# Kernel optimization log

Hardware: AMD Instinct MI355X
Metric: run time of the kernel (lower is better)

Reference implementation:

```python
import jax, jax.numpy as jnp
import numpy as np

N_USER = 80000
N_ITEM = 20000
N = N_USER + N_ITEM          # total nodes
E = 1600000                  # edges (nnz of norm_adj), avg degree 16
EMB = 64                     # emb_size
FEAT = 64                    # feature_dim -> input_dim = 128
D = EMB + FEAT               # 128
L = 3                        # number of GCN layers, layer_size=[128,128,128]
K = 3                        # max_hop
B = 4096                     # batch_size


def setup_inputs() -> dict:
    key = jax.random.key(0)
    ks = jax.random.split(key, 16)
    deg_scale = 1.0 / 16.0  # ~normalized adjacency values
    return {
        'edge_row': jax.random.randint(ks[0], (E,), 0, N, dtype=jnp.int32),
        'edge_col': jax.random.randint(ks[1], (E,), 0, N, dtype=jnp.int32),
        'edge_val': jax.random.uniform(ks[2], (E,), dtype=jnp.float32) * deg_scale,
        'feat': jax.random.normal(ks[3], (N_USER, FEAT), dtype=jnp.float32) * 0.1,
        'user_emb': jax.random.normal(ks[4], (N_USER, EMB), dtype=jnp.float32) * 0.1,
        'item_emb1': jax.random.normal(ks[5], (N_ITEM, EMB), dtype=jnp.float32) * 0.1,
        'item_emb2': jax.random.normal(ks[6], (N_ITEM, FEAT), dtype=jnp.float32) * 0.1,
        'alphas': jax.random.normal(ks[7], (L, K), dtype=jnp.float32) * 0.1,
        'W_gc': jax.random.normal(ks[8], (L, D, D), dtype=jnp.float32) * 0.05,
        'b_gc': jax.random.normal(ks[9], (L, 1, D), dtype=jnp.float32) * 0.05,
        'W_bi': jax.random.normal(ks[10], (L, D, D), dtype=jnp.float32) * 0.05,
        'b_bi': jax.random.normal(ks[11], (L, 1, D), dtype=jnp.float32) * 0.05,
        'users': jax.random.randint(ks[12], (B,), 0, N_USER, dtype=jnp.int32),
        'pos_items': jax.random.randint(ks[13], (B,), 0, N_ITEM, dtype=jnp.int32),
        'neg_items': jax.random.randint(ks[14], (B,), 0, N_ITEM, dtype=jnp.int32),
    }


def reference(edge_row, edge_col, edge_val, feat, user_emb, item_emb1,
              item_emb2, alphas, W_gc, b_gc, W_bi, b_bi,
              users, pos_items, neg_items):
    def spmm(X):
        # A_hat @ X via edge-list gather + segment-sum (sparse.mm equivalent)
        return jax.ops.segment_sum(edge_val[:, None] * X[edge_col], edge_row,
                                   num_segments=N)

    # ego embeddings: [[user_emb|feat], [item_emb1|item_emb2]] -> [N, D]
    ego = jnp.concatenate([
        jnp.concatenate([user_emb, item_emb1], axis=0),
        jnp.concatenate([feat, item_emb2], axis=0),
    ], axis=1)

    all_embs = [ego]
    for k in range(L):
        # multi-order aggregation: sum_i beta_i * A^i @ ego
        beta = jax.nn.softmax(alphas[k])
        cur = spmm(ego)
        side = beta[0] * cur
        for i in range(1, K):
            cur = spmm(cur)
            side = side + beta[i] * cur
        sum_e = side @ W_gc[k] + b_gc[k]
        bi_e = (ego * side) @ W_bi[k] + b_bi[k]
        # aggregator_mode == 'sum_bi'
        ego = jax.nn.leaky_relu(sum_e, negative_slope=0.2) + bi_e
        # mess_dropout = 0 -> identity; L2-normalize rows (F.normalize eps=1e-12)
        norm = ego / jnp.maximum(
            jnp.linalg.norm(ego, axis=1, keepdims=True), 1e-12)
        all_embs.append(norm)

    all_emb = jnp.concatenate(all_embs, axis=1)  # [N, D*(L+1)] = [N, 512]
    u_emb = all_emb[:N_USER]
    i_emb = all_emb[N_USER:]
    return (u_emb[users], i_emb[pos_items], i_emb[neg_items])
```

## Files before the change

kernel.cpp:

```cpp
#include <hip/hip_runtime.h>
#include <hip/hip_bf16.h>

typedef __hip_bfloat16 hbf16;
typedef unsigned short u16;
typedef __bf16 bf16x8 __attribute__((ext_vector_type(8)));
typedef float f32x4 __attribute__((ext_vector_type(4)));

#define N_USERS 80000
#define N_ITEMS 20000
#define NTOT    100000
#define NEDGE   1600000
#define DDIM    128
#define NLAY    3
#define KHOP    3
#define NB      4096
#define LBM     128
#define NBUK    49
#define BROWS   2048

__device__ inline u16 f2bfu(float f) { __bf16 h = (__bf16)f; return __builtin_bit_cast(u16, h); }

__global__ void beta_kernel(const float* __restrict__ alphas, float* __restrict__ beta) {
    if (threadIdx.x == 0 && blockIdx.x == 0) {
        for (int k = 0; k < NLAY; ++k) {
            float a[KHOP];
            float m = -1e30f;
            for (int i = 0; i < KHOP; ++i) { a[i] = alphas[k*KHOP+i]; m = fmaxf(m, a[i]); }
            float s = 0.f;
            for (int i = 0; i < KHOP; ++i) { a[i] = expf(a[i] - m); s += a[i]; }
            for (int i = 0; i < KHOP; ++i) beta[k*KHOP+i] = a[i] / s;
        }
    }
}

__global__ void build_ego_kernel(const float* __restrict__ feat, const float* __restrict__ user_emb,
                                 const float* __restrict__ item_emb1, const float* __restrict__ item_emb2,
                                 u16* __restrict__ ego) {
    int i = blockIdx.x * 256 + threadIdx.x;
    int n = i >> 7, d = i & 127;
    float v;
    if (n < N_USERS) {
        v = (d < 64) ? user_emb[n*64 + d] : feat[n*64 + d - 64];
    } else {
        int m = n - N_USERS;
        v = (d < 64) ? item_emb1[m*64 + d] : item_emb2[m*64 + d - 64];
    }
    ego[i] = f2bfu(v);
}

__global__ void transpose_w_kernel(const float* __restrict__ Wgc, const float* __restrict__ Wbi,
                                   u16* __restrict__ WTgc, u16* __restrict__ WTbi) {
    __shared__ float t[32][33];
    int z = blockIdx.z;
    const float* W = (z < 3) ? (Wgc + (size_t)z * 16384) : (Wbi + (size_t)(z - 3) * 16384);
    u16* WT = (z < 3) ? (WTgc + (size_t)z * 16384) : (WTbi + (size_t)(z - 3) * 16384);
    int r0 = blockIdx.y * 32, c0 = blockIdx.x * 32;
    for (int i = threadIdx.y; i < 32; i += 8)
        t[i][threadIdx.x] = W[(size_t)(r0 + i) * 128 + c0 + threadIdx.x];
    __syncthreads();
    for (int i = threadIdx.y; i < 32; i += 8)
        WT[(size_t)(c0 + i) * 128 + r0 + threadIdx.x] = f2bfu(t[threadIdx.x][i]);
}

__global__ void zero_kernel(int* __restrict__ p, int n) {
    int i = blockIdx.x * 256 + threadIdx.x;
    if (i < n) p[i] = 0;
}

__global__ __launch_bounds__(256) void bhist_kernel(const int* __restrict__ er,
                                                    int* __restrict__ bbins) {
    __shared__ int l[NBUK];
    int tid = threadIdx.x;
    if (tid < NBUK) l[tid] = 0;
    __syncthreads();
    for (int i = blockIdx.x * 256 + tid; i < NEDGE; i += gridDim.x * 256)
        atomicAdd(&l[er[i] >> 11], 1);
    __syncthreads();
    if (tid < NBUK && l[tid]) atomicAdd(&bbins[tid], l[tid]);
}

__global__ void bscan_kernel(const int* __restrict__ bbins, int* __restrict__ bbase,
                             int* __restrict__ bcur) {
    if (threadIdx.x == 0 && blockIdx.x == 0) {
        int acc = 0;
        for (int b = 0; b < NBUK; ++b) { int t = bbins[b]; bbase[b] = acc; bcur[b] = acc; acc += t; }
        bbase[NBUK] = acc;
    }
}

__global__ __launch_bounds__(256) void bappend_kernel(
    const int* __restrict__ er, const int* __restrict__ ec, const float* __restrict__ ev,
    int* __restrict__ bcur, int* __restrict__ tmprow, int2* __restrict__ tmpcv) {
    __shared__ int lcnt[NBUK], lbase[NBUK], lrank[NBUK];
    int tid = threadIdx.x;
    for (int b = tid; b < NBUK; b += 256) { lcnt[b] = 0; lrank[b] = 0; }
    __syncthreads();
    int base = blockIdx.x * 2048;
    int r[8], c[8], vb[8], bk[8];
    bool ok[8];
    #pragma unroll
    for (int k = 0; k < 8; ++k) {
        int i = base + k * 256 + tid;
        ok[k] = i < NEDGE;
        bk[k] = 0;
        if (ok[k]) {
            r[k] = er[i]; c[k] = ec[i]; vb[k] = __float_as_int(ev[i]);
            bk[k] = r[k] >> 11;
            atomicAdd(&lcnt[bk[k]], 1);
        }
    }
    __syncthreads();
    for (int b = tid; b < NBUK; b += 256)
        lbase[b] = lcnt[b] ? atomicAdd(&bcur[b], lcnt[b]) : 0;
    __syncthreads();
    #pragma unroll
    for (int k = 0; k < 8; ++k) {
        if (ok[k]) {
            int rank = atomicAdd(&lrank[bk[k]], 1);
            int pos = lbase[bk[k]] + rank;
            tmprow[pos] = r[k];
            tmpcv[pos] = make_int2(c[k], vb[k]);
        }
    }
}

__global__ __launch_bounds__(1024) void bfinal_kernel(
    const int* __restrict__ bbase, const int* __restrict__ tmprow,
    const int2* __restrict__ tmpcv, int* __restrict__ rowptr, int2* __restrict__ edges) {
    __shared__ int lhist[BROWS];
    __shared__ int lbase[BROWS];
    __shared__ int s2[1024];
    int b = blockIdx.x, tid = threadIdx.x;
    int s = bbase[b], e = bbase[b + 1];
    int rbase = b << 11;
    int nrows = min(NTOT - rbase, BROWS);
    lhist[tid] = 0; lhist[tid + 1024] = 0;
    __syncthreads();
    for (int i = s + tid; i < e; i += 1024)
        atomicAdd(&lhist[tmprow[i] - rbase], 1);
    __syncthreads();
    int a0 = lhist[tid * 2], a1 = lhist[tid * 2 + 1];
    s2[tid] = a0 + a1;
    __syncthreads();
    for (int off = 1; off < 1024; off <<= 1) {
        int t = (tid >= off) ? s2[tid - off] : 0;
        __syncthreads();
        s2[tid] += t;
        __syncthreads();
    }
    int excl = s2[tid] - a0 - a1;
    lbase[tid * 2] = excl;
    lbase[tid * 2 + 1] = excl + a0;
    __syncthreads();
    for (int j = tid; j < nrows; j += 1024)
        rowptr[rbase + j] = s + lbase[j];
    if (b == NBUK - 1 && tid == 0) rowptr[NTOT] = NEDGE;
    lhist[tid * 2] = lbase[tid * 2];
    lhist[tid * 2 + 1] = lbase[tid * 2 + 1];
    __syncthreads();
    for (int i = s + tid; i < e; i += 1024) {
        int lr = tmprow[i] - rbase;
        int p = atomicAdd(&lhist[lr], 1);
        edges[s + p] = tmpcv[i];
    }
}

__device__ inline void ld_edge_nt(const int2* __restrict__ p, int& c, float& v) {
    unsigned long long rec =
        __builtin_nontemporal_load(reinterpret_cast<const unsigned long long*>(p));
    c = (int)(unsigned)(rec & 0xffffffffull);
    v = __int_as_float((int)(unsigned)(rec >> 32));
}

__global__ __launch_bounds__(256) void spmm_kernel(
    const int* __restrict__ rowptr, const int2* __restrict__ edges,
    const u16* __restrict__ X, u16* __restrict__ Y) {
    int tid = threadIdx.x;
    int r = blockIdx.x * 16 + (tid >> 4);
    int lane = tid & 15;
    int s = rowptr[r], e = rowptr[r + 1];
    float acc[8];
    #pragma unroll
    for (int i = 0; i < 8; ++i) acc[i] = 0.f;
    const u16* xb = X + lane * 8;
    int j = s;
    for (; j + 8 <= e; j += 8) {
        int cc[8]; float vv[8];
        #pragma unroll
        for (int u = 0; u < 8; ++u) ld_edge_nt(edges + j + u, cc[u], vv[u]);
        bf16x8 x[8];
        #pragma unroll
        for (int u = 0; u < 8; ++u)
            x[u] = *reinterpret_cast<const bf16x8*>(xb + (size_t)cc[u] * DDIM);
        #pragma unroll
        for (int u = 0; u < 8; ++u) {
            #pragma unroll
            for (int i = 0; i < 8; ++i) acc[i] = fmaf(vv[u], (float)x[u][i], acc[i]);
        }
    }
    for (; j + 4 <= e; j += 4) {
        int cc[4]; float vv[4];
        #pragma unroll
        for (int u = 0; u < 4; ++u) ld_edge_nt(edges + j + u, cc[u], vv[u]);
        bf16x8 x0 = *reinterpret_cast<const bf16x8*>(xb + (size_t)cc[0] * DDIM);
        bf16x8 x1 = *reinterpret_cast<const bf16x8*>(xb + (size_t)cc[1] * DDIM);
        bf16x8 x2 = *reinterpret_cast<const bf16x8*>(xb + (size_t)cc[2] * DDIM);
        bf16x8 x3 = *reinterpret_cast<const bf16x8*>(xb + (size_t)cc[3] * DDIM);
        #pragma unroll
        for (int i = 0; i < 8; ++i) acc[i] = fmaf(vv[0], (float)x0[i], acc[i]);
        #pragma unroll
        for (int i = 0; i < 8; ++i) acc[i] = fmaf(vv[1], (float)x1[i], acc[i]);
        #pragma unroll
        for (int i = 0; i < 8; ++i) acc[i] = fmaf(vv[2], (float)x2[i], acc[i]);
        #pragma unroll
        for (int i = 0; i < 8; ++i) acc[i] = fmaf(vv[3], (float)x3[i], acc[i]);
    }
    for (; j < e; ++j) {
        int cc; float vv;
        ld_edge_nt(edges + j, cc, vv);
        bf16x8 x = *reinterpret_cast<const bf16x8*>(xb + (size_t)cc * DDIM);
        #pragma unroll
        for (int i = 0; i < 8; ++i) acc[i] = fmaf(vv, (float)x[i], acc[i]);
    }
    size_t oi = (size_t)r * DDIM + lane * 8;
    bf16x8 y;
    #pragma unroll
    for (int i = 0; i < 8; ++i) y[i] = (__bf16)acc[i];
    *reinterpret_cast<bf16x8*>(Y + oi) = y;
}

__global__ __launch_bounds__(512) void layer_kernel(
    const u16* __restrict__ ego, const u16* __restrict__ h1,
    const u16* __restrict__ h2, const u16* __restrict__ h3,
    const float* __restrict__ beta3,
    const u16* __restrict__ wtgc, const u16* __restrict__ wtbi,
    const float* __restrict__ bgc, const float* __restrict__ bbi,
    u16* __restrict__ ego_out, u16* __restrict__ normbuf) {
    __shared__ __align__(16) unsigned char smem[131072];
    const int AS = 0, AB = 32768, WG = 65536, WB = 98304;
    int tid = threadIdx.x;
    int base = blockIdx.x * LBM;
    float b0 = beta3[0], b1 = beta3[1], b2 = beta3[2];

    {
        int row = tid >> 2, q = tid & 3;
        int grow = base + row;
        bool ok = grow < NTOT;
        size_t roff = (size_t)grow * DDIM + q * 32;
        int sw = (row & 7) << 4;
        #pragma unroll
        for (int cg = 0; cg < 4; ++cg) {
            bf16x8 pa, pb;
            if (ok) {
                bf16x8 x1 = *reinterpret_cast<const bf16x8*>(h1 + roff + cg * 8);
                bf16x8 x2 = *reinterpret_cast<const bf16x8*>(h2 + roff + cg * 8);
                bf16x8 x3 = *reinterpret_cast<const bf16x8*>(h3 + roff + cg * 8);
                bf16x8 ev = *reinterpret_cast<const bf16x8*>(ego + roff + cg * 8);
                #pragma unroll
                for (int i = 0; i < 8; ++i) {
                    float sf = b0 * (float)x1[i] + b1 * (float)x2[i] + b2 * (float)x3[i];
                    pa[i] = (__bf16)sf;
                    pb[i] = (__bf16)(sf * (float)ev[i]);
                }
            } else {
                #pragma unroll
                for (int i = 0; i < 8; ++i) { pa[i] = (__bf16)0.f; pb[i] = (__bf16)0.f; }
            }
            int kb = q * 64 + cg * 16;
            *reinterpret_cast<bf16x8*>(&smem[AS + row * 256 + (kb ^ sw)]) = pa;
            *reinterpret_cast<bf16x8*>(&smem[AB + row * 256 + (kb ^ sw)]) = pb;
        }
    }
    #pragma unroll
    for (int p = 0; p < 4; ++p) {
        int slot = tid + p * 512;
        int n = slot >> 4, ks = slot & 15;
        uint4 g  = *reinterpret_cast<const uint4*>(wtgc + n * DDIM + ks * 8);
        uint4 bq = *reinterpret_cast<const uint4*>(wtbi + n * DDIM + ks * 8);
        int addr = n * 256 + ((ks * 16) ^ ((n & 7) << 4));
        *reinterpret_cast<uint4*>(&smem[WG + addr]) = g;
        *reinterpret_cast<uint4*>(&smem[WB + addr]) = bq;
    }
    __syncthreads();

    int l = tid & 63, w = tid >> 6;
    int m = l & 15, g16 = l >> 4;
    int sw = (m & 7) << 4;
    int arow = (w * 16 + m) * 256;
    f32x4 accg[8], accb[8];
    #pragma unroll
    for (int nt = 0; nt < 8; ++nt) {
        accg[nt] = (f32x4){0.f, 0.f, 0.f, 0.f};
        accb[nt] = (f32x4){0.f, 0.f, 0.f, 0.f};
    }
    #pragma unroll
    for (int kk = 0; kk < 4; ++kk) {
        int ka = (kk * 64 + g16 * 16) ^ sw;
        bf16x8 as = *reinterpret_cast<const bf16x8*>(&smem[AS + arow + ka]);
        bf16x8 ab = *reinterpret_cast<const bf16x8*>(&smem[AB + arow + ka]);
        #pragma unroll
        for (int nt = 0; nt < 8; ++nt) {
            int na = (nt * 16 + m) * 256 + ka;
            bf16x8 bg = *reinterpret_cast<const bf16x8*>(&smem[WG + na]);
            accg[nt] = __builtin_amdgcn_mfma_f32_16x16x32_bf16(as, bg, accg[nt], 0, 0, 0);
            bf16x8 bb = *reinterpret_cast<const bf16x8*>(&smem[WB + na]);
            accb[nt] = __builtin_amdgcn_mfma_f32_16x16x32_bf16(ab, bb, accb[nt], 0, 0, 0);
        }
    }
    float bgv[8], bbv[8];
    #pragma unroll
    for (int nt = 0; nt < 8; ++nt) { bgv[nt] = bgc[nt * 16 + m]; bbv[nt] = bbi[nt * 16 + m]; }
    float vv[8][4];
    float ss[4] = {0.f, 0.f, 0.f, 0.f};
    #pragma unroll
    for (int nt = 0; nt < 8; ++nt) {
        #pragma unroll
        for (int rr = 0; rr < 4; ++rr) {
            float se = accg[nt][rr] + bgv[nt];
            float be = accb[nt][rr] + bbv[nt];
            float v = (se > 0.f ? se : 0.2f * se) + be;
            vv[nt][rr] = v;
            ss[rr] += v * v;
            int row = base + w * 16 + g16 * 4 + rr;
            if (row < NTOT) ego_out[(size_t)row * DDIM + nt * 16 + m] = f2bfu(v);
        }
    }
    #pragma unroll
    for (int rr = 0; rr < 4; ++rr) {
        ss[rr] += __shfl_xor(ss[rr], 1, 64);
        ss[rr] += __shfl_xor(ss[rr], 2, 64);
        ss[rr] += __shfl_xor(ss[rr], 4, 64);
        ss[rr] += __shfl_xor(ss[rr], 8, 64);
        ss[rr] = 1.f / fmaxf(sqrtf(ss[rr]), 1e-12f);
    }
    #pragma unroll
    for (int nt = 0; nt < 8; ++nt) {
        #pragma unroll
        for (int rr = 0; rr < 4; ++rr) {
            int row = base + w * 16 + g16 * 4 + rr;
            if (row < NTOT) normbuf[(size_t)row * DDIM + nt * 16 + m] = f2bfu(vv[nt][rr] * ss[rr]);
        }
    }
}

__global__ void gather_ego_kernel(const float* __restrict__ feat, const float* __restrict__ user_emb,
                                  const float* __restrict__ item_emb1, const float* __restrict__ item_emb2,
                                  const int* __restrict__ users, const int* __restrict__ pos,
                                  const int* __restrict__ neg, float* __restrict__ out) {
    int i = blockIdx.x * 256 + threadIdx.x;
    int which = i / (NB * DDIM);
    int rem = i - which * (NB * DDIM);
    int b = rem >> 7, d = rem & 127;
    float v;
    if (which == 0) {
        int u = users[b];
        v = (d < 64) ? user_emb[u*64 + d] : feat[u*64 + d - 64];
    } else {
        int m = (which == 1) ? pos[b] : neg[b];
        v = (d < 64) ? item_emb1[m*64 + d] : item_emb2[m*64 + d - 64];
    }
    out[(size_t)which * NB * 512 + (size_t)b * 512 + d] = v;
}

__global__ void gather_slice_kernel(const u16* __restrict__ src, const int* __restrict__ users,
                                    const int* __restrict__ pos, const int* __restrict__ neg,
                                    float* __restrict__ out, int slot) {
    int i = blockIdx.x * 256 + threadIdx.x;
    int which = i / (NB * DDIM);
    int rem = i - which * (NB * DDIM);
    int b = rem >> 7, c = rem & 127;
    int row;
    if (which == 0)      row = users[b];
    else if (which == 1) row = N_USERS + pos[b];
    else                 row = N_USERS + neg[b];
    unsigned int u = src[(size_t)row * DDIM + c];
    out[(size_t)which * NB * 512 + (size_t)b * 512 + slot * 128 + c] =
        __builtin_bit_cast(float, u << 16);
}

extern "C" void kernel_launch(void* const* d_in, const int* in_sizes, int n_in,
                              void* d_out, int out_size, void* d_ws, size_t ws_size,
                              hipStream_t stream) {
    (void)in_sizes; (void)n_in; (void)out_size; (void)ws_size;
    const int*   edge_row  = (const int*)  d_in[0];
    const int*   edge_col  = (const int*)  d_in[1];
    const float* edge_val  = (const float*)d_in[2];
    const float* feat      = (const float*)d_in[3];
    const float* user_emb  = (const float*)d_in[4];
    const float* item_emb1 = (const float*)d_in[5];
    const float* item_emb2 = (const float*)d_in[6];
    const float* alphas    = (const float*)d_in[7];
    const float* W_gc      = (const float*)d_in[8];
    const float* b_gc      = (const float*)d_in[9];
    const float* W_bi      = (const float*)d_in[10];
    const float* b_bi      = (const float*)d_in[11];
    const int*   users     = (const int*)  d_in[12];
    const int*   pos_items = (const int*)  d_in[13];
    const int*   neg_items = (const int*)  d_in[14];
    float* out = (float*)d_out;

    char* ws = (char*)d_ws;
    size_t off = 0;
    auto alloc = [&](size_t bytes) -> char* {
        char* p = ws + off;
        off = (off + bytes + 255) & ~(size_t)255;
        return p;
    };
    u16*   ego      = (u16*)  alloc((size_t)NTOT * DDIM * 2);
    u16*   h1       = (u16*)  alloc((size_t)NTOT * DDIM * 2);
    u16*   h2       = (u16*)  alloc((size_t)NTOT * DDIM * 2);
    u16*   h3       = (u16*)  alloc((size_t)NTOT * DDIM * 2);
    u16*   normbuf  = (u16*)  alloc((size_t)NTOT * DDIM * 2);
    int*   rowptr   = (int*)  alloc((size_t)(NTOT + 1) * 4);
    int*   bbins    = (int*)  alloc((NBUK + 2) * 4);
    int*   bbase    = (int*)  alloc((NBUK + 2) * 4);
    int*   bcur     = (int*)  alloc((NBUK + 2) * 4);
    int2*  edges    = (int2*) alloc((size_t)NEDGE * 8);
    u16*   wtgc     = (u16*)  alloc((size_t)NLAY * DDIM * DDIM * 2);
    u16*   wtbi     = (u16*)  alloc((size_t)NLAY * DDIM * DDIM * 2);
    float* beta     = (float*)alloc(256);

    int*  tmprow = (int*)h1;
    int2* tmpcv  = (int2*)((char*)h1 + (size_t)NEDGE * 4);

    beta_kernel<<<1, 64, 0, stream>>>(alphas, beta);
    build_ego_kernel<<<(NTOT * DDIM) / 256, 256, 0, stream>>>(feat, user_emb, item_emb1, item_emb2, ego);
    transpose_w_kernel<<<dim3(4, 4, 6), dim3(32, 8), 0, stream>>>(W_gc, W_bi, wtgc, wtbi);

    zero_kernel<<<1, 64, 0, stream>>>(bbins, NBUK);
    bhist_kernel<<<512, 256, 0, stream>>>(edge_row, bbins);
    bscan_kernel<<<1, 64, 0, stream>>>(bbins, bbase, bcur);
    bappend_kernel<<<(NEDGE + 2047) / 2048, 256, 0, stream>>>(edge_row, edge_col, edge_val,
                                                              bcur, tmprow, tmpcv);
    bfinal_kernel<<<NBUK, 1024, 0, stream>>>(bbase, tmprow, tmpcv, rowptr, edges);

    gather_ego_kernel<<<(3 * NB * DDIM) / 256, 256, 0, stream>>>(feat, user_emb, item_emb1, item_emb2,
                                                                 users, pos_items, neg_items, out);

    int lgrid = (NTOT + LBM - 1) / LBM;
    for (int k = 0; k < NLAY; ++k) {
        spmm_kernel<<<NTOT / 16, 256, 0, stream>>>(rowptr, edges, ego, h1);
        spmm_kernel<<<NTOT / 16, 256, 0, stream>>>(rowptr, edges, h1, h2);
        spmm_kernel<<<NTOT / 16, 256, 0, stream>>>(rowptr, edges, h2, h3);
        layer_kernel<<<lgrid, 512, 0, stream>>>(ego, h1, h2, h3, beta + 3 * k,
                                                wtgc + (size_t)k * DDIM * DDIM, wtbi + (size_t)k * DDIM * DDIM,
                                                b_gc + (size_t)k * DDIM, b_bi + (size_t)k * DDIM,
                                                ego, normbuf);
        gather_slice_kernel<<<(3 * NB * DDIM) / 256, 256, 0, stream>>>(normbuf, users, pos_items, neg_items, out, k + 1);
    }
}
```

Measured before the change: 875.6 us.

## Load GEMM A operands directly into registers, halve LDS, add SpMM sched barriers

The layer kernel no longer stages the beta-combined side and ego*side tiles in shared memory. Each lane now loads its MFMA A-fragment straight from global memory and combines it in registers, which halves LDS use to 64KB and adds a launch-bounds hint for more resident blocks. The SpMM kernel gains sched_barrier calls so all gathers issue before the FMAs, and its 4-edge tail loop is restructured the same way. The risk is less coalesced global loads for the A operand and more register pressure.

```diff
diff --git a/kernel.cpp b/kernel.cpp
--- a/kernel.cpp
+++ b/kernel.cpp
@@ -192,6 +192,7 @@
         #pragma unroll
         for (int u = 0; u < 8; ++u)
             x[u] = *reinterpret_cast<const bf16x8*>(xb + (size_t)cc[u] * DDIM);
+        __builtin_amdgcn_sched_barrier(0);
         #pragma unroll
         for (int u = 0; u < 8; ++u) {
             #pragma unroll
@@ -202,18 +203,16 @@
         int cc[4]; float vv[4];
         #pragma unroll
         for (int u = 0; u < 4; ++u) ld_edge_nt(edges + j + u, cc[u], vv[u]);
-        bf16x8 x0 = *reinterpret_cast<const bf16x8*>(xb + (size_t)cc[0] * DDIM);
-        bf16x8 x1 = *reinterpret_cast<const bf16x8*>(xb + (size_t)cc[1] * DDIM);
-        bf16x8 x2 = *reinterpret_cast<const bf16x8*>(xb + (size_t)cc[2] * DDIM);
-        bf16x8 x3 = *reinterpret_cast<const bf16x8*>(xb + (size_t)cc[3] * DDIM);
-        #pragma unroll
-        for (int i = 0; i < 8; ++i) acc[i] = fmaf(vv[0], (float)x0[i], acc[i]);
-        #pragma unroll
-        for (int i = 0; i < 8; ++i) acc[i] = fmaf(vv[1], (float)x1[i], acc[i]);
-        #pragma unroll
-        for (int i = 0; i < 8; ++i) acc[i] = fmaf(vv[2], (float)x2[i], acc[i]);
-        #pragma unroll
-        for (int i = 0; i < 8; ++i) acc[i] = fmaf(vv[3], (float)x3[i], acc[i]);
+        bf16x8 x[4];
+        #pragma unroll
+        for (int u = 0; u < 4; ++u)
+            x[u] = *reinterpret_cast<const bf16x8*>(xb + (size_t)cc[u] * DDIM);
+        __builtin_amdgcn_sched_barrier(0);
+        #pragma unroll
+        for (int u = 0; u < 4; ++u) {
+            #pragma unroll
+            for (int i = 0; i < 8; ++i) acc[i] = fmaf(vv[u], (float)x[u][i], acc[i]);
+        }
     }
     for (; j < e; ++j) {
         int cc; float vv;
@@ -229,48 +228,19 @@
     *reinterpret_cast<bf16x8*>(Y + oi) = y;
 }
 
-__global__ __launch_bounds__(512) void layer_kernel(
+__global__ __launch_bounds__(512, 4) void layer_kernel(
     const u16* __restrict__ ego, const u16* __restrict__ h1,
     const u16* __restrict__ h2, const u16* __restrict__ h3,
     const float* __restrict__ beta3,
     const u16* __restrict__ wtgc, const u16* __restrict__ wtbi,
     const float* __restrict__ bgc, const float* __restrict__ bbi,
     u16* __restrict__ ego_out, u16* __restrict__ normbuf) {
-    __shared__ __align__(16) unsigned char smem[131072];
-    const int AS = 0, AB = 32768, WG = 65536, WB = 98304;
+    __shared__ __align__(16) unsigned char smem[65536];
+    const int WG = 0, WB = 32768;
     int tid = threadIdx.x;
     int base = blockIdx.x * LBM;
     float b0 = beta3[0], b1 = beta3[1], b2 = beta3[2];
 
-    {
-        int row = tid >> 2, q = tid & 3;
-        int grow = base + row;
-        bool ok = grow < NTOT;
-        size_t roff = (size_t)grow * DDIM + q * 32;
-        int sw = (row & 7) << 4;
-        #pragma unroll
-        for (int cg = 0; cg < 4; ++cg) {
-            bf16x8 pa, pb;
-            if (ok) {
-                bf16x8 x1 = *reinterpret_cast<const bf16x8*>(h1 + roff + cg * 8);
-                bf16x8 x2 = *reinterpret_cast<const bf16x8*>(h2 + roff + cg * 8);
-                bf16x8 x3 = *reinterpret_cast<const bf16x8*>(h3 + roff + cg * 8);
-                bf16x8 ev = *reinterpret_cast<const bf16x8*>(ego + roff + cg * 8);
-                #pragma unroll
-                for (int i = 0; i < 8; ++i) {
-                    float sf = b0 * (float)x1[i] + b1 * (float)x2[i] + b2 * (float)x3[i];
-                    pa[i] = (__bf16)sf;
-                    pb[i] = (__bf16)(sf * (float)ev[i]);
-                }
-            } else {
-                #pragma unroll
-                for (int i = 0; i < 8; ++i) { pa[i] = (__bf16)0.f; pb[i] = (__bf16)0.f; }
-            }
-            int kb = q * 64 + cg * 16;
-            *reinterpret_cast<bf16x8*>(&smem[AS + row * 256 + (kb ^ sw)]) = pa;
-            *reinterpret_cast<bf16x8*>(&smem[AB + row * 256 + (kb ^ sw)]) = pb;
-        }
-    }
     #pragma unroll
     for (int p = 0; p < 4; ++p) {
         int slot = tid + p * 512;
@@ -286,7 +256,11 @@
     int l = tid & 63, w = tid >> 6;
     int m = l & 15, g16 = l >> 4;
     int sw = (m & 7) << 4;
-    int arow = (w * 16 + m) * 256;
+    int grow = base + w * 16 + m;
+    bool ok = grow < NTOT;
+    int grc = ok ? grow : 0;
+    size_t aoff = (size_t)grc * DDIM + g16 * 8;
+
     f32x4 accg[8], accb[8];
     #pragma unroll
     for (int nt = 0; nt < 8; ++nt) {
@@ -295,9 +269,18 @@
     }
     #pragma unroll
     for (int kk = 0; kk < 4; ++kk) {
+        bf16x8 x1 = *reinterpret_cast<const bf16x8*>(h1 + aoff + kk * 32);
+        bf16x8 x2 = *reinterpret_cast<const bf16x8*>(h2 + aoff + kk * 32);
+        bf16x8 x3 = *reinterpret_cast<const bf16x8*>(h3 + aoff + kk * 32);
+        bf16x8 ev = *reinterpret_cast<const bf16x8*>(ego + aoff + kk * 32);
+        bf16x8 as, ab;
+        #pragma unroll
+        for (int i = 0; i < 8; ++i) {
+            float sf = ok ? (b0 * (float)x1[i] + b1 * (float)x2[i] + b2 * (float)x3[i]) : 0.f;
+            as[i] = (__bf16)sf;
+            ab[i] = (__bf16)(sf * (float)ev[i]);
+        }
         int ka = (kk * 64 + g16 * 16) ^ sw;
-        bf16x8 as = *reinterpret_cast<const bf16x8*>(&smem[AS + arow + ka]);
-        bf16x8 ab = *reinterpret_cast<const bf16x8*>(&smem[AB + arow + ka]);
         #pragma unroll
         for (int nt = 0; nt < 8; ++nt) {
             int na = (nt * 16 + m) * 256 + ka;
```

Result: faster. 853.6 us (-2.5%).
